# Kernel tuning notes

Measured on AMD Instinct MI355X. Metric: run time of the kernel, lower is better.

Reference implementation:

```python
import jax, jax.numpy as jnp
import numpy as np
from functools import partial

DG = 16          # deform groups
KH = KW = 3      # deformable kernel
K = KH * KW
MAX_MAG = 10.0   # max_residue_magnitude


def conv3x3(x, w, b):
    # x: [B,C,H,W], w: [O,C,3,3]
    y = jax.lax.conv_general_dilated(
        x, w, window_strides=(1, 1), padding=((1, 1), (1, 1)),
        dimension_numbers=('NCHW', 'OIHW', 'NCHW'))
    return y + b[None, :, None, None]


def lrelu(v):
    return jnp.where(v >= 0, v, 0.1 * v)


def modulated_deform_conv2d(x, offset, mask, weight, bias):
    """torchvision.ops.deform_conv2d semantics, stride=1, pad=1, dil=1, groups=1.
    x: [B,C,H,W]; offset: [B,2*DG*K,H,W] as (dy,dx) pairs; mask: [B,DG*K,H,W];
    weight: [Cout,C,KH,KW]; bias: [Cout]."""
    B, C, H, W = x.shape
    Cout = weight.shape[0]
    Ho, Wo = H, W  # stride 1, pad 1, 3x3
    Cp = C // DG

    off = offset.reshape(B, DG, K, 2, Ho, Wo)
    dy, dx = off[:, :, :, 0], off[:, :, :, 1]          # [B,DG,K,Ho,Wo]

    ki = (jnp.arange(K) // KW).astype(jnp.float32)      # kernel row
    kj = (jnp.arange(K) % KW).astype(jnp.float32)       # kernel col
    base_i = jnp.arange(Ho, dtype=jnp.float32) - 1.0    # i*stride - pad
    base_j = jnp.arange(Wo, dtype=jnp.float32) - 1.0
    py = dy + base_i[None, None, None, :, None] + ki[None, None, :, None, None]
    px = dx + base_j[None, None, None, None, :] + kj[None, None, :, None, None]

    y0 = jnp.floor(py)
    x0 = jnp.floor(px)
    wy = py - y0   # frac parts
    wx = px - x0
    y0i = y0.astype(jnp.int32)
    x0i = x0.astype(jnp.int32)

    xg = x.reshape(B, DG, Cp, H * W)
    P = K * Ho * Wo

    def gather(yi, xi, wgt):
        valid = (yi >= 0) & (yi < H) & (xi >= 0) & (xi < W)
        yc = jnp.clip(yi, 0, H - 1)
        xc = jnp.clip(xi, 0, W - 1)
        idx = (yc * W + xc).reshape(B, DG, 1, P)
        v = jnp.take_along_axis(xg, idx, axis=3)          # [B,DG,Cp,P]
        w = (wgt * valid.astype(x.dtype)).reshape(B, DG, 1, P)
        return v * w

    acc = gather(y0i,     x0i,     (1 - wy) * (1 - wx))
    acc = acc + gather(y0i,     x0i + 1, (1 - wy) * wx)
    acc = acc + gather(y0i + 1, x0i,     wy * (1 - wx))
    acc = acc + gather(y0i + 1, x0i + 1, wy * wx)

    acc = acc * mask.reshape(B, DG, 1, P)                 # modulation
    cols = acc.reshape(B, C, K, Ho * Wo)                  # [B,C,K,HW]
    out = jnp.einsum('ock,bckp->bop', weight.reshape(Cout, C, K), cols)
    out = out + bias[None, :, None]
    return out.reshape(B, Cout, Ho, Wo)


def forward(x, cond, flow, w1, b1, w2, b2, w3, b3, w4, b4, weight, bias):
    h = lrelu(conv3x3(cond, w1, b1))
    h = lrelu(conv3x3(h, w2, b2))
    h = lrelu(conv3x3(h, w3, b3))
    out = conv3x3(h, w4, b4)                              # [B,27*DG,H,W]
    offset, mask = out[:, :18 * DG], out[:, 18 * DG:]
    offset = MAX_MAG * jnp.tanh(offset)
    # flow channels are (dx,dy); flip -> (dy,dx) matching offset pair layout
    rep = offset.shape[1] // 2
    offset = offset + jnp.tile(flow[:, ::-1], (1, rep, 1, 1))
    mask = jax.nn.sigmoid(mask)
    return modulated_deform_conv2d(x, offset, mask, weight, bias)


def setup_inputs() -> dict:
    key = jax.random.key(0)
    ks = jax.random.split(key, 16)
    B, C, H, W = 2, 64, 128, 128
    Cc = 2 * C + 5  # 133
    s = 0.05
    return {
        'x': jax.random.normal(ks[0], (B, C, H, W), jnp.float32),
        'cond': jax.random.normal(ks[1], (B, Cc, H, W), jnp.float32),
        'flow': jax.random.normal(ks[2], (B, 2, H, W), jnp.float32),
        'w1': jax.random.normal(ks[3], (C, Cc, 3, 3), jnp.float32) * s,
        'b1': jax.random.normal(ks[4], (C,), jnp.float32) * s,
        'w2': jax.random.normal(ks[5], (C, C, 3, 3), jnp.float32) * s,
        'b2': jax.random.normal(ks[6], (C,), jnp.float32) * s,
        'w3': jax.random.normal(ks[7], (C, C, 3, 3), jnp.float32) * s,
        'b3': jax.random.normal(ks[8], (C,), jnp.float32) * s,
        'w4': jax.random.normal(ks[9], (27 * DG, C, 3, 3), jnp.float32) * s,
        'b4': jax.random.normal(ks[10], (27 * DG,), jnp.float32) * s,
        'weight': jax.random.normal(ks[11], (C, C, 3, 3), jnp.float32) * s,
        'bias': jax.random.normal(ks[12], (C,), jnp.float32) * s,
    }


def reference(x, cond, flow, w1, b1, w2, b2, w3, b3, w4, b4, weight, bias):
    return forward(x, cond, flow, w1, b1, w2, b2, w3, b3, w4, b4, weight, bias)
```

## Files before the change

### kernel.cpp

```cpp
#include <hip/hip_runtime.h>
#include <math.h>

#define Hh 128
#define Ww 128
#define HW (128*128)
#define PITCH 130
#define PADPX (130*130)

typedef unsigned short u16;
typedef unsigned int uint;
typedef _Float16 f16;
typedef __attribute__((ext_vector_type(8))) _Float16 f16x8;
typedef __attribute__((ext_vector_type(4))) _Float16 f16x4;
typedef __attribute__((ext_vector_type(4))) float f32x4;

__global__ __launch_bounds__(256) void zero_edge_k(u16* __restrict__ buf, int cu16) {
  int per_px = cu16 >> 3;
  int total = 516 * per_px;
  int idx = blockIdx.x * 256 + threadIdx.x;
  int b = blockIdx.y;
  if (idx >= total) return;
  int e = idx / per_px, q = idx - e * per_px;
  int y, x;
  if (e < 130)      { y = 0;   x = e; }
  else if (e < 260) { y = 129; x = e - 130; }
  else { int j = e - 260; y = 1 + (j >> 1); x = (j & 1) ? 129 : 0; }
  *(uint4*)&buf[((size_t)b * PADPX + (size_t)(y * PITCH + x)) * cu16 + q * 8] =
      make_uint4(0, 0, 0, 0);
}

__global__ __launch_bounds__(256) void prep_cond_k(const float* __restrict__ cond,
                                                   f16* __restrict__ out) {
  int p = blockIdx.x * 256 + threadIdx.x;
  int b = blockIdx.y;
  int y = p >> 7, x = p & 127;
  const float* cb = cond + (size_t)b * 133 * HW + p;
  f16* ob = out + ((size_t)b * PADPX + (size_t)((y + 1) * PITCH + x + 1)) * 160;
  for (int c = 0; c < 160; c += 8) {
    f16 buf[8];
    #pragma unroll
    for (int j = 0; j < 8; j++) {
      float v = (c + j < 133) ? cb[(size_t)(c + j) * HW] : 0.f;
      buf[j] = (f16)v;
    }
    *(uint4*)&ob[c] = *(uint4*)buf;
  }
}

__global__ __launch_bounds__(256) void wtrans_mfma_k(const float* __restrict__ w,
                                                     f16* __restrict__ wt,
                                                     int CIN, int NC, int NCOF) {
  int idx = blockIdx.x * 256 + threadIdx.x;
  int total = 9 * NC * NCOF * 64;
  if (idx >= total) return;
  int lane = idx & 63;
  int frag = idx >> 6;
  int f = frag % NCOF;
  int rest = frag / NCOF;
  int c = rest % NC;
  int t = rest / NC;
  int co = f * 16 + (lane & 15);
  int ci0 = c * 32 + (lane >> 4) * 8;
  f16 buf[8];
  #pragma unroll
  for (int j = 0; j < 8; j++) {
    int ci = ci0 + j;
    buf[j] = (f16)((ci < CIN) ? w[((size_t)co * CIN + ci) * 9 + t] : 0.f);
  }
  *(uint4*)&wt[(size_t)idx * 8] = *(uint4*)buf;
}

__global__ __launch_bounds__(256) void wtrans_dcn_mfma_k(const float* __restrict__ w,
                                                         f16* __restrict__ wt) {
  int idx = blockIdx.x * 256 + threadIdx.x;
  if (idx >= 18 * 4 * 64) return;
  int lane = idx & 63;
  int frag = idx >> 6;
  int f = frag & 3;
  int chunk = frag >> 2;
  int co = f * 16 + (lane & 15);
  int ci0 = chunk * 32 + (lane >> 4) * 8;
  f16 buf[8];
  #pragma unroll
  for (int j = 0; j < 8; j++) {
    int ci = ci0 + j;
    int k = ci >> 6, cig = ci & 63;
    buf[j] = (f16)w[((size_t)co * 64 + cig) * 9 + k];
  }
  *(uint4*)&wt[(size_t)idx * 8] = *(uint4*)buf;
}

__global__ __launch_bounds__(256) void xtrans2_k(const float* __restrict__ x,
                                                 f16* __restrict__ xt2, int B) {
  int idx = blockIdx.x * 256 + threadIdx.x;
  int total = B * 16 * HW;
  if (idx >= total) return;
  int b = idx / (16 * HW);
  int r = idx % (16 * HW);
  int dg = r / HW, p = r % HW;
  int y = p >> 7, xx = p & 127;
  int x1 = min(xx + 1, 127);
  const float* xb = x + ((size_t)b * 64 + dg * 4) * HW + (size_t)y * Ww;
  f16 o[8];
  #pragma unroll
  for (int c = 0; c < 4; c++) {
    o[c] = (f16)xb[(size_t)c * HW + xx];
    o[4 + c] = (f16)xb[(size_t)c * HW + x1];
  }
  *(uint4*)&xt2[(size_t)idx * 8] = *(uint4*)o;
}

template<int CINP, int NC, int NCF, int NCOF, int EPI>
__global__ __launch_bounds__(256) void conv_f16_k(
    const f16* __restrict__ in, const f16* __restrict__ wt,
    const float* __restrict__ bias, f16* __restrict__ out,
    float* __restrict__ offb, f16* __restrict__ mskb,
    const float* __restrict__ flow, int cogroups)
{
  __shared__ u16 lds[180 * 40];
  const int tid = threadIdx.x;
  const int lane = tid & 63, wave = tid >> 6;
  const int b = blockIdx.z / cogroups, cog = blockIdx.z % cogroups;
  const int gx0 = blockIdx.x * 16, gy0 = blockIdx.y * 8;

  f32x4 acc[2][NCF];
  #pragma unroll
  for (int i = 0; i < 2; i++)
    #pragma unroll
    for (int j = 0; j < NCF; j++) acc[i][j] = (f32x4)0.f;

  const f16* inb = in + (size_t)b * PADPX * CINP;

  for (int c = 0; c < NC; c++) {
    __syncthreads();
    for (int i = tid; i < 720; i += 256) {
      int pidx = i >> 2, q = i & 3;
      int py = pidx / 18, px = pidx - py * 18;
      size_t gp = (size_t)((gy0 + py) * PITCH + gx0 + px);
      uint4 v = *(const uint4*)&inb[gp * CINP + c * 32 + q * 8];
      *(uint4*)&lds[pidx * 40 + q * 8] = v;
    }
    __syncthreads();

    #pragma unroll
    for (int tap = 0; tap < 9; tap++) {
      const int dy = tap / 3, dx = tap % 3;
      f16x8 bfrag[2];
      #pragma unroll
      for (int pl = 0; pl < 2; pl++) {
        int pidx_r = (wave * 2 + pl + dy) * 18 + (lane & 15) + dx;
        bfrag[pl] = *(const f16x8*)&lds[pidx_r * 40 + (lane >> 4) * 8];
      }
      const f16* fA = wt + (((size_t)(tap * NC + c)) * NCOF + cog * NCF) * 512
                      + (size_t)lane * 8;
      #pragma unroll
      for (int cf = 0; cf < NCF; cf++) {
        f16x8 a = *(const f16x8*)&fA[(size_t)cf * 512];
        #pragma unroll
        for (int pl = 0; pl < 2; pl++)
          acc[pl][cf] = __builtin_amdgcn_mfma_f32_16x16x32_f16(a, bfrag[pl], acc[pl][cf], 0, 0, 0);
      }
    }
  }

  const int co_l = (lane >> 4) * 4;
  if (EPI == 0) {
    #pragma unroll
    for (int pl = 0; pl < 2; pl++) {
      size_t pp = (size_t)((gy0 + wave * 2 + pl + 1) * PITCH + gx0 + (lane & 15) + 1);
      f16* ob = out + ((size_t)b * PADPX + pp) * (NCOF * 16);
      #pragma unroll
      for (int cf = 0; cf < NCF; cf++) {
        int c0 = (cog * NCF + cf) * 16 + co_l;
        f16 buf[4];
        #pragma unroll
        for (int r = 0; r < 4; r++) {
          float v = acc[pl][cf][r] + bias[c0 + r];
          buf[r] = (f16)((v >= 0.f) ? v : 0.1f * v);
        }
        *(uint2*)&ob[c0] = *(uint2*)buf;
      }
    }
  } else {
    #pragma unroll
    for (int pl = 0; pl < 2; pl++) {
      size_t pix = (size_t)(gy0 + wave * 2 + pl) * Ww + gx0 + (lane & 15);
      float fl0 = flow[((size_t)b * 2 + 0) * HW + pix];
      float fl1 = flow[((size_t)b * 2 + 1) * HW + pix];
      #pragma unroll
      for (int cf = 0; cf < NCF; cf++) {
        int c0 = (cog * NCF + cf) * 16 + co_l;
        #pragma unroll
        for (int r = 0; r < 4; r++) {
          int cc = c0 + r;
          float v = acc[pl][cf][r] + bias[cc];
          if (cc < 288) {
            float e = __expf(2.f * v);
            float t = 1.f - 2.f * __builtin_amdgcn_rcpf(e + 1.f);
            offb[((size_t)b * 288 + cc) * HW + pix] = 10.f * t + ((cc & 1) ? fl0 : fl1);
          } else {
            mskb[((size_t)b * 144 + (cc - 288)) * HW + pix] =
                (f16)__builtin_amdgcn_rcpf(1.f + __expf(-v));
          }
        }
      }
    }
  }
}

__global__ __launch_bounds__(256) void dcn_fused_k(
    const f16* __restrict__ xt2, const float* __restrict__ off,
    const f16* __restrict__ msk, const f16* __restrict__ wtd,
    const float* __restrict__ bias, float* __restrict__ out)
{
  __shared__ u16 buf[2][64][72];
  const int tid = threadIdx.x;
  const int lane = tid & 63, wave = tid >> 6;
  const int bid = blockIdx.x;
  const int nid = (bid & 7) * 64 + (bid >> 3);
  const int b = nid >> 8;
  const int px0 = (nid & 255) * 64;
  const int pxl = tid & 63;
  const int px = px0 + pxl;
  const int y = px >> 7, x0i = px & 127;
  const int dg2 = tid >> 6;

  const float* offp = off + (size_t)b * 288 * HW + px;
  const f16*   mp   = msk + (size_t)b * 144 * HW + px;
  const f16*   xpl  = xt2 + (size_t)(b * 16 + dg2 * 4) * ((size_t)HW * 8);

  f32x4 acc[4];
  #pragma unroll
  for (int f = 0; f < 4; f++) acc[f] = (f32x4)0.f;

  float dyv[2][4], dxv[2][4], mvv[2][4];
  f16x8 g0[4], g1[4];
  float w00[4], w01[4], w10[4], w11[4];
  int hsel[4];

#define OFF_LOAD(kk, sl) { \
  _Pragma("unroll") \
  for (int i = 0; i < 4; i++) { int dg = dg2 * 4 + i; \
    dyv[sl][i] = offp[(size_t)(dg * 18 + 2 * (kk)) * HW]; \
    dxv[sl][i] = offp[(size_t)(dg * 18 + 2 * (kk) + 1) * HW]; \
    mvv[sl][i] = (float)mp[(size_t)(dg * 9 + (kk)) * HW]; } }

#define GATHER(kk, sl) { \
  _Pragma("unroll") \
  for (int i = 0; i < 4; i++) { \
    float py = (float)(y - 1 + (kk) / 3) + dyv[sl][i]; \
    float pxx = (float)(x0i - 1 + (kk) % 3) + dxv[sl][i]; \
    float y0f = floorf(py), x0f = floorf(pxx); \
    float wy = py - y0f, wx = pxx - x0f; \
    int yi = (int)y0f, xi = (int)x0f; \
    bool vy0 = (yi >= 0) & (yi < Hh); \
    bool vy1 = (yi + 1 >= 0) & (yi + 1 < Hh); \
    bool vx0 = (xi >= 0) & (xi < Ww); \
    bool vx1 = (xi + 1 >= 0) & (xi + 1 < Ww); \
    int y0c = min(max(yi, 0), Hh - 1), y1c = min(max(yi + 1, 0), Hh - 1); \
    int xb = min(max(xi, 0), Ww - 1); \
    hsel[i] = min(max(xi + 1, 0), Ww - 1) - xb; \
    float mv = mvv[sl][i]; \
    w00[i] = (vy0 && vx0) ? (1.f - wy) * (1.f - wx) * mv : 0.f; \
    w01[i] = (vy0 && vx1) ? (1.f - wy) * wx * mv : 0.f; \
    w10[i] = (vy1 && vx0) ? wy * (1.f - wx) * mv : 0.f; \
    w11[i] = (vy1 && vx1) ? wy * wx * mv : 0.f; \
    const f16* xp = xpl + (size_t)i * ((size_t)HW * 8); \
    g0[i] = *(const f16x8*)&xp[(size_t)(y0c * Ww + xb) * 8]; \
    g1[i] = *(const f16x8*)&xp[(size_t)(y1c * Ww + xb) * 8]; } }

#define FIN(nb) { \
  f16 o[16]; \
  _Pragma("unroll") \
  for (int i = 0; i < 4; i++) { \
    _Pragma("unroll") \
    for (int c = 0; c < 4; c++) { \
      float a00 = (float)g0[i][c]; \
      float a01 = hsel[i] ? (float)g0[i][4 + c] : (float)g0[i][c]; \
      float a10 = (float)g1[i][c]; \
      float a11 = hsel[i] ? (float)g1[i][4 + c] : (float)g1[i][c]; \
      o[i * 4 + c] = (f16)(a00 * w00[i] + a01 * w01[i] + a10 * w10[i] + a11 * w11[i]); } } \
  *(uint4*)&buf[nb][pxl][dg2 * 16] = *(uint4*)&o[0]; \
  *(uint4*)&buf[nb][pxl][dg2 * 16 + 8] = *(uint4*)&o[8]; }

#define MFMA_TAP(kk) { \
  _Pragma("unroll") \
  for (int ch = 0; ch < 2; ch++) { \
    f16x8 bfr = *(const f16x8*)&buf[(kk) & 1][wave * 16 + (lane & 15)][(lane >> 4) * 8 + ch * 32]; \
    const f16* wc = wtd + ((size_t)(((kk) * 2 + ch) * 4) * 64 + (size_t)lane) * 8; \
    _Pragma("unroll") \
    for (int f = 0; f < 4; f++) { \
      f16x8 a = *(const f16x8*)&wc[(size_t)f * 512]; \
      acc[f] = __builtin_amdgcn_mfma_f32_16x16x32_f16(a, bfr, acc[f], 0, 0, 0); } } }

  OFF_LOAD(0, 0);
  GATHER(0, 0);
  OFF_LOAD(1, 1);
  FIN(0);
  __syncthreads();

  #pragma unroll
  for (int k = 0; k < 9; k++) {
    if (k < 8) { GATHER(k + 1, (k + 1) & 1); }
    if (k < 7) { OFF_LOAD(k + 2, k & 1); }
    MFMA_TAP(k);
    if (k < 8) { FIN((k + 1) & 1); }
    __syncthreads();
  }

  const int pxo = px0 + wave * 16 + (lane & 15);
  #pragma unroll
  for (int f = 0; f < 4; f++) {
    #pragma unroll
    for (int r = 0; r < 4; r++) {
      int co = f * 16 + (lane >> 4) * 4 + r;
      out[((size_t)b * 64 + co) * HW + pxo] = acc[f][r] + bias[co];
    }
  }
#undef OFF_LOAD
#undef GATHER
#undef FIN
#undef MFMA_TAP
}

extern "C" void kernel_launch(void* const* d_in, const int* in_sizes, int n_in,
                              void* d_out, int out_size, void* d_ws, size_t ws_size,
                              hipStream_t stream) {
  const float* x    = (const float*)d_in[0];
  const float* cond = (const float*)d_in[1];
  const float* flow = (const float*)d_in[2];
  const float* w1 = (const float*)d_in[3];
  const float* b1 = (const float*)d_in[4];
  const float* w2 = (const float*)d_in[5];
  const float* b2 = (const float*)d_in[6];
  const float* w3 = (const float*)d_in[7];
  const float* b3 = (const float*)d_in[8];
  const float* w4 = (const float*)d_in[9];
  const float* b4 = (const float*)d_in[10];
  const float* wD = (const float*)d_in[11];
  const float* bD = (const float*)d_in[12];
  float* out = (float*)d_out;
  const int B = 2;

  char* ws = (char*)d_ws;
  f16* condp = (f16*)ws;
  f16* hA = (f16*)(ws + 10816000);
  f16* hB = (f16*)(ws + 15142400);
  char* pw = ws + 19468800;
  float* offb = (float*)pw;          pw += 37748736;
  f16*   mskb = (f16*)pw;            pw += 9437184;
  f16*   xt2  = (f16*)pw;            pw += 8388608;
  f16*   wt1  = (f16*)pw;            pw += 184320;
  f16*   wt2  = (f16*)pw;            pw += 73728;
  f16*   wt3  = (f16*)pw;            pw += 73728;
  f16*   wt4  = (f16*)pw;            pw += 497664;
  f16*   wtd  = (f16*)pw;            pw += 73728;

  zero_edge_k<<<dim3((516 * 20 + 255) / 256, B), 256, 0, stream>>>((u16*)condp, 160);
  zero_edge_k<<<dim3((516 * 8 + 255) / 256, B), 256, 0, stream>>>((u16*)hA, 64);
  zero_edge_k<<<dim3((516 * 8 + 255) / 256, B), 256, 0, stream>>>((u16*)hB, 64);
  prep_cond_k<<<dim3(HW / 256, B), 256, 0, stream>>>(cond, condp);
  xtrans2_k<<<dim3(B * 16 * HW / 256), 256, 0, stream>>>(x, xt2, B);
  wtrans_mfma_k<<<dim3((9 * 5 * 4 * 64 + 255) / 256), 256, 0, stream>>>(w1, wt1, 133, 5, 4);
  wtrans_mfma_k<<<dim3((9 * 2 * 4 * 64 + 255) / 256), 256, 0, stream>>>(w2, wt2, 64, 2, 4);
  wtrans_mfma_k<<<dim3((9 * 2 * 4 * 64 + 255) / 256), 256, 0, stream>>>(w3, wt3, 64, 2, 4);
  wtrans_mfma_k<<<dim3((9 * 2 * 27 * 64 + 255) / 256), 256, 0, stream>>>(w4, wt4, 64, 2, 27);
  wtrans_dcn_mfma_k<<<dim3((18 * 4 * 64 + 255) / 256), 256, 0, stream>>>(wD, wtd);

  conv_f16_k<160, 5, 1, 4, 0><<<dim3(8, 16, B * 4), 256, 0, stream>>>(
      condp, wt1, b1, hA, nullptr, nullptr, nullptr, 4);
  conv_f16_k<64, 2, 1, 4, 0><<<dim3(8, 16, B * 4), 256, 0, stream>>>(
      hA, wt2, b2, hB, nullptr, nullptr, nullptr, 4);
  conv_f16_k<64, 2, 1, 4, 0><<<dim3(8, 16, B * 4), 256, 0, stream>>>(
      hB, wt3, b3, hA, nullptr, nullptr, nullptr, 4);
  conv_f16_k<64, 2, 3, 27, 2><<<dim3(8, 16, B * 9), 256, 0, stream>>>(
      hA, wt4, b4, nullptr, offb, mskb, flow, 9);

  dcn_fused_k<<<dim3(512), 256, 0, stream>>>(xt2, offb, mskb, wtd, bD, out);
}
```

Baseline: 149.3 us.

## Prefetch conv input tiles into registers and repartition DCN over smaller pixel tiles

The conv kernel now loads the next channel chunk's input tile into registers while the current chunk is computed, then writes it to LDS after the barrier. This overlaps global-load latency with the MFMA work. The fused deformable conv is repartitioned so each block handles 16 pixels, with one thread per (pixel, deform group) and each wave owning 16 output channels. That gives 4x more blocks, fewer registers per thread and a higher occupancy hint. In exchange, each block reloads the DCN weights over fewer pixels, and the output stores become narrower.

```diff
diff --git a/kernel.cpp b/kernel.cpp
--- a/kernel.cpp
+++ b/kernel.cpp
@@ -131,15 +131,31 @@
 
   const f16* inb = in + (size_t)b * PADPX * CINP;
 
+  uint4 rbuf[3];
+#define LOADC(cc) { \
+    if (tid < 240) { \
+      _Pragma("unroll") \
+      for (int j = 0; j < 3; j++) { \
+        int i = j * 240 + tid; \
+        int pidx = i >> 2, q = i & 3; \
+        int py = pidx / 18, px = pidx - py * 18; \
+        size_t gp = (size_t)((gy0 + py) * PITCH + gx0 + px); \
+        rbuf[j] = *(const uint4*)&inb[gp * CINP + (cc) * 32 + q * 8]; \
+      } } }
+#define WRITEC() { \
+    if (tid < 240) { \
+      _Pragma("unroll") \
+      for (int j = 0; j < 3; j++) { \
+        int i = j * 240 + tid; \
+        int pidx = i >> 2, q = i & 3; \
+        *(uint4*)&lds[pidx * 40 + q * 8] = rbuf[j]; \
+      } } }
+
+  LOADC(0);
   for (int c = 0; c < NC; c++) {
     __syncthreads();
-    for (int i = tid; i < 720; i += 256) {
-      int pidx = i >> 2, q = i & 3;
-      int py = pidx / 18, px = pidx - py * 18;
-      size_t gp = (size_t)((gy0 + py) * PITCH + gx0 + px);
-      uint4 v = *(const uint4*)&inb[gp * CINP + c * 32 + q * 8];
-      *(uint4*)&lds[pidx * 40 + q * 8] = v;
-    }
+    WRITEC();
+    if (c + 1 < NC) LOADC(c + 1);
     __syncthreads();
 
     #pragma unroll
@@ -162,6 +178,8 @@
       }
     }
   }
+#undef LOADC
+#undef WRITEC
 
   const int co_l = (lane >> 4) * 4;
   if (EPI == 0) {
@@ -208,48 +226,42 @@
   }
 }
 
-__global__ __launch_bounds__(256) void dcn_fused_k(
+__global__ __launch_bounds__(256, 8) void dcn_fused_k(
     const f16* __restrict__ xt2, const float* __restrict__ off,
     const f16* __restrict__ msk, const f16* __restrict__ wtd,
     const float* __restrict__ bias, float* __restrict__ out)
 {
-  __shared__ u16 buf[2][64][72];
+  __shared__ u16 buf[2][16][72];
   const int tid = threadIdx.x;
   const int lane = tid & 63, wave = tid >> 6;
   const int bid = blockIdx.x;
-  const int nid = (bid & 7) * 64 + (bid >> 3);
-  const int b = nid >> 8;
-  const int px0 = (nid & 255) * 64;
-  const int pxl = tid & 63;
+  const int nid = (bid & 7) * 256 + (bid >> 3);
+  const int b = nid >> 10;
+  const int px0 = (nid & 1023) * 16;
+  const int pxl = tid & 15;
+  const int dg  = tid >> 4;
   const int px = px0 + pxl;
   const int y = px >> 7, x0i = px & 127;
-  const int dg2 = tid >> 6;
 
   const float* offp = off + (size_t)b * 288 * HW + px;
   const f16*   mp   = msk + (size_t)b * 144 * HW + px;
-  const f16*   xpl  = xt2 + (size_t)(b * 16 + dg2 * 4) * ((size_t)HW * 8);
-
-  f32x4 acc[4];
-  #pragma unroll
-  for (int f = 0; f < 4; f++) acc[f] = (f32x4)0.f;
-
-  float dyv[2][4], dxv[2][4], mvv[2][4];
-  f16x8 g0[4], g1[4];
-  float w00[4], w01[4], w10[4], w11[4];
-  int hsel[4];
+  const f16*   xp   = xt2 + (size_t)(b * 16 + dg) * ((size_t)HW * 8);
+
+  f32x4 acc = (f32x4)0.f;
+
+  float dyv[2], dxv[2], mvv[2];
+  f16x8 g0, g1;
+  float w00, w01, w10, w11;
+  int hsel;
 
 #define OFF_LOAD(kk, sl) { \
-  _Pragma("unroll") \
-  for (int i = 0; i < 4; i++) { int dg = dg2 * 4 + i; \
-    dyv[sl][i] = offp[(size_t)(dg * 18 + 2 * (kk)) * HW]; \
-    dxv[sl][i] = offp[(size_t)(dg * 18 + 2 * (kk) + 1) * HW]; \
-    mvv[sl][i] = (float)mp[(size_t)(dg * 9 + (kk)) * HW]; } }
+    dyv[sl] = offp[(size_t)(dg * 18 + 2 * (kk)) * HW]; \
+    dxv[sl] = offp[(size_t)(dg * 18 + 2 * (kk) + 1) * HW]; \
+    mvv[sl] = (float)mp[(size_t)(dg * 9 + (kk)) * HW]; }
 
 #define GATHER(kk, sl) { \
-  _Pragma("unroll") \
-  for (int i = 0; i < 4; i++) { \
-    float py = (float)(y - 1 + (kk) / 3) + dyv[sl][i]; \
-    float pxx = (float)(x0i - 1 + (kk) % 3) + dxv[sl][i]; \
+    float py = (float)(y - 1 + (kk) / 3) + dyv[sl]; \
+    float pxx = (float)(x0i - 1 + (kk) % 3) + dxv[sl]; \
     float y0f = floorf(py), x0f = floorf(pxx); \
     float wy = py - y0f, wx = pxx - x0f; \
     int yi = (int)y0f, xi = (int)x0f; \
@@ -259,39 +271,33 @@
     bool vx1 = (xi + 1 >= 0) & (xi + 1 < Ww); \
     int y0c = min(max(yi, 0), Hh - 1), y1c = min(max(yi + 1, 0), Hh - 1); \
     int xb = min(max(xi, 0), Ww - 1); \
-    hsel[i] = min(max(xi + 1, 0), Ww - 1) - xb; \
-    float mv = mvv[sl][i]; \
-    w00[i] = (vy0 && vx0) ? (1.f - wy) * (1.f - wx) * mv : 0.f; \
-    w01[i] = (vy0 && vx1) ? (1.f - wy) * wx * mv : 0.f; \
-    w10[i] = (vy1 && vx0) ? wy * (1.f - wx) * mv : 0.f; \
-    w11[i] = (vy1 && vx1) ? wy * wx * mv : 0.f; \
-    const f16* xp = xpl + (size_t)i * ((size_t)HW * 8); \
-    g0[i] = *(const f16x8*)&xp[(size_t)(y0c * Ww + xb) * 8]; \
-    g1[i] = *(const f16x8*)&xp[(size_t)(y1c * Ww + xb) * 8]; } }
+    hsel = min(max(xi + 1, 0), Ww - 1) - xb; \
+    float mv = mvv[sl]; \
+    w00 = (vy0 && vx0) ? (1.f - wy) * (1.f - wx) * mv : 0.f; \
+    w01 = (vy0 && vx1) ? (1.f - wy) * wx * mv : 0.f; \
+    w10 = (vy1 && vx0) ? wy * (1.f - wx) * mv : 0.f; \
+    w11 = (vy1 && vx1) ? wy * wx * mv : 0.f; \
+    g0 = *(const f16x8*)&xp[(size_t)(y0c * Ww + xb) * 8]; \
+    g1 = *(const f16x8*)&xp[(size_t)(y1c * Ww + xb) * 8]; }
 
 #define FIN(nb) { \
-  f16 o[16]; \
-  _Pragma("unroll") \
-  for (int i = 0; i < 4; i++) { \
+    f16 o[4]; \
     _Pragma("unroll") \
     for (int c = 0; c < 4; c++) { \
-      float a00 = (float)g0[i][c]; \
-      float a01 = hsel[i] ? (float)g0[i][4 + c] : (float)g0[i][c]; \
-      float a10 = (float)g1[i][c]; \
-      float a11 = hsel[i] ? (float)g1[i][4 + c] : (float)g1[i][c]; \
-      o[i * 4 + c] = (f16)(a00 * w00[i] + a01 * w01[i] + a10 * w10[i] + a11 * w11[i]); } } \
-  *(uint4*)&buf[nb][pxl][dg2 * 16] = *(uint4*)&o[0]; \
-  *(uint4*)&buf[nb][pxl][dg2 * 16 + 8] = *(uint4*)&o[8]; }
+      float a00 = (float)g0[c]; \
+      float a01 = hsel ? (float)g0[4 + c] : (float)g0[c]; \
+      float a10 = (float)g1[c]; \
+      float a11 = hsel ? (float)g1[4 + c] : (float)g1[c]; \
+      o[c] = (f16)(a00 * w00 + a01 * w01 + a10 * w10 + a11 * w11); } \
+    *(uint2*)&buf[nb][pxl][dg * 4] = *(uint2*)o; }
 
 #define MFMA_TAP(kk) { \
-  _Pragma("unroll") \
-  for (int ch = 0; ch < 2; ch++) { \
-    f16x8 bfr = *(const f16x8*)&buf[(kk) & 1][wave * 16 + (lane & 15)][(lane >> 4) * 8 + ch * 32]; \
-    const f16* wc = wtd + ((size_t)(((kk) * 2 + ch) * 4) * 64 + (size_t)lane) * 8; \
     _Pragma("unroll") \
-    for (int f = 0; f < 4; f++) { \
-      f16x8 a = *(const f16x8*)&wc[(size_t)f * 512]; \
-      acc[f] = __builtin_amdgcn_mfma_f32_16x16x32_f16(a, bfr, acc[f], 0, 0, 0); } } }
+    for (int ch = 0; ch < 2; ch++) { \
+      f16x8 bfr = *(const f16x8*)&buf[(kk) & 1][lane & 15][(lane >> 4) * 8 + ch * 32]; \
+      const f16* wc = wtd + ((size_t)((((kk) * 2 + ch) * 4 + wave)) * 64 + (size_t)lane) * 8; \
+      f16x8 a = *(const f16x8*)wc; \
+      acc = __builtin_amdgcn_mfma_f32_16x16x32_f16(a, bfr, acc, 0, 0, 0); } }
 
   OFF_LOAD(0, 0);
   GATHER(0, 0);
@@ -308,14 +314,11 @@
     __syncthreads();
   }
 
-  const int pxo = px0 + wave * 16 + (lane & 15);
-  #pragma unroll
-  for (int f = 0; f < 4; f++) {
-    #pragma unroll
-    for (int r = 0; r < 4; r++) {
-      int co = f * 16 + (lane >> 4) * 4 + r;
-      out[((size_t)b * 64 + co) * HW + pxo] = acc[f][r] + bias[co];
-    }
+  const int pxo = px0 + (lane & 15);
+  #pragma unroll
+  for (int r = 0; r < 4; r++) {
+    int co = wave * 16 + (lane >> 4) * 4 + r;
+    out[((size_t)b * 64 + co) * HW + pxo] = acc[r] + bias[co];
   }
 #undef OFF_LOAD
 #undef GATHER
@@ -376,5 +379,5 @@
   conv_f16_k<64, 2, 3, 27, 2><<<dim3(8, 16, B * 9), 256, 0, stream>>>(
       hA, wt4, b4, nullptr, offb, mskb, flow, 9);
 
-  dcn_fused_k<<<dim3(512), 256, 0, stream>>>(xt2, offb, mskb, wtd, bD, out);
-}
+  dcn_fused_k<<<dim3(2048), 256, 0, stream>>>(xt2, offb, mskb, wtd, bD, out);
+}
```

Result: slower. 187.0 us (+25.3%).

## Merge prep kernels into two launches and stage two channel chunks per sync

Applied to the files above, without the earlier changes.

Folds the edge-zeroing, cond and x transpose kernels into one prep launch, and the five weight-transform kernels into a second, cutting eight small launches. The conv kernel now loads two 32-channel chunks into shared memory per barrier pair, which halves the syncs for the 64-channel convs. The cost is double the LDS per block, which may lower occupancy, plus extra index arithmetic in the merged kernels.

```diff
diff --git a/kernel.cpp b/kernel.cpp
--- a/kernel.cpp
+++ b/kernel.cpp
@@ -11,113 +11,127 @@
 typedef unsigned int uint;
 typedef _Float16 f16;
 typedef __attribute__((ext_vector_type(8))) _Float16 f16x8;
-typedef __attribute__((ext_vector_type(4))) _Float16 f16x4;
 typedef __attribute__((ext_vector_type(4))) float f32x4;
 
-__global__ __launch_bounds__(256) void zero_edge_k(u16* __restrict__ buf, int cu16) {
-  int per_px = cu16 >> 3;
-  int total = 516 * per_px;
+__global__ __launch_bounds__(256) void prep_all_k(
+    const float* __restrict__ cond, const float* __restrict__ x,
+    f16* __restrict__ condp, f16* __restrict__ hA, f16* __restrict__ hB,
+    f16* __restrict__ xt2)
+{
+  int t = blockIdx.x * 256 + threadIdx.x;
+  if (t < 32768) {
+    int b = t >> 14, p = t & 16383;
+    int y = p >> 7, xx = p & 127;
+    const float* cb = cond + (size_t)b * 133 * HW + p;
+    f16* ob = condp + ((size_t)b * PADPX + (size_t)((y + 1) * PITCH + xx + 1)) * 160;
+    for (int c = 0; c < 160; c += 8) {
+      f16 buf[8];
+      #pragma unroll
+      for (int j = 0; j < 8; j++) {
+        float v = (c + j < 133) ? cb[(size_t)(c + j) * HW] : 0.f;
+        buf[j] = (f16)v;
+      }
+      *(uint4*)&ob[c] = *(uint4*)buf;
+    }
+    return;
+  }
+  t -= 32768;
+  if (t < 20640) {
+    int b = t / 10320, i = t % 10320;
+    int e = i / 20, q = i % 20;
+    int y, xx;
+    if (e < 130)      { y = 0;   xx = e; }
+    else if (e < 260) { y = 129; xx = e - 130; }
+    else { int j = e - 260; y = 1 + (j >> 1); xx = (j & 1) ? 129 : 0; }
+    *(uint4*)&condp[((size_t)b * PADPX + (size_t)(y * PITCH + xx)) * 160 + q * 8] =
+        make_uint4(0, 0, 0, 0);
+    return;
+  }
+  t -= 20640;
+  if (t < 16512) {
+    f16* buf = (t < 8256) ? hA : hB;
+    int i = t % 8256;
+    int b = i / 4128; i %= 4128;
+    int e = i / 8, q = i % 8;
+    int y, xx;
+    if (e < 130)      { y = 0;   xx = e; }
+    else if (e < 260) { y = 129; xx = e - 130; }
+    else { int j = e - 260; y = 1 + (j >> 1); xx = (j & 1) ? 129 : 0; }
+    *(uint4*)&buf[((size_t)b * PADPX + (size_t)(y * PITCH + xx)) * 64 + q * 8] =
+        make_uint4(0, 0, 0, 0);
+    return;
+  }
+  t -= 16512;
+  if (t < 524288) {
+    int b = t / (16 * HW);
+    int r = t % (16 * HW);
+    int dg = r / HW, p = r % HW;
+    int y = p >> 7, xx = p & 127;
+    int x1 = min(xx + 1, 127);
+    const float* xb = x + ((size_t)b * 64 + dg * 4) * HW + (size_t)y * Ww;
+    f16 o[8];
+    #pragma unroll
+    for (int c = 0; c < 4; c++) {
+      o[c] = (f16)xb[(size_t)c * HW + xx];
+      o[4 + c] = (f16)xb[(size_t)c * HW + x1];
+    }
+    *(uint4*)&xt2[(size_t)t * 8] = *(uint4*)o;
+  }
+}
+
+__global__ __launch_bounds__(256) void wtrans_all_k(
+    const float* __restrict__ w1, const float* __restrict__ w2,
+    const float* __restrict__ w3, const float* __restrict__ w4,
+    const float* __restrict__ wD,
+    f16* __restrict__ wt1, f16* __restrict__ wt2, f16* __restrict__ wt3,
+    f16* __restrict__ wt4, f16* __restrict__ wtd)
+{
   int idx = blockIdx.x * 256 + threadIdx.x;
-  int b = blockIdx.y;
-  if (idx >= total) return;
-  int e = idx / per_px, q = idx - e * per_px;
-  int y, x;
-  if (e < 130)      { y = 0;   x = e; }
-  else if (e < 260) { y = 129; x = e - 130; }
-  else { int j = e - 260; y = 1 + (j >> 1); x = (j & 1) ? 129 : 0; }
-  *(uint4*)&buf[((size_t)b * PADPX + (size_t)(y * PITCH + x)) * cu16 + q * 8] =
-      make_uint4(0, 0, 0, 0);
-}
-
-__global__ __launch_bounds__(256) void prep_cond_k(const float* __restrict__ cond,
-                                                   f16* __restrict__ out) {
-  int p = blockIdx.x * 256 + threadIdx.x;
-  int b = blockIdx.y;
-  int y = p >> 7, x = p & 127;
-  const float* cb = cond + (size_t)b * 133 * HW + p;
-  f16* ob = out + ((size_t)b * PADPX + (size_t)((y + 1) * PITCH + x + 1)) * 160;
-  for (int c = 0; c < 160; c += 8) {
+  if (idx >= 882 * 64) return;
+  int lane = idx & 63;
+  int fid = idx >> 6;
+  if (fid >= 810) {
+    int f2 = fid - 810;
+    int f = f2 & 3, chunk = f2 >> 2;
+    int co = f * 16 + (lane & 15);
+    int ci0 = chunk * 32 + (lane >> 4) * 8;
     f16 buf[8];
     #pragma unroll
     for (int j = 0; j < 8; j++) {
-      float v = (c + j < 133) ? cb[(size_t)(c + j) * HW] : 0.f;
-      buf[j] = (f16)v;
-    }
-    *(uint4*)&ob[c] = *(uint4*)buf;
-  }
-}
-
-__global__ __launch_bounds__(256) void wtrans_mfma_k(const float* __restrict__ w,
-                                                     f16* __restrict__ wt,
-                                                     int CIN, int NC, int NCOF) {
-  int idx = blockIdx.x * 256 + threadIdx.x;
-  int total = 9 * NC * NCOF * 64;
-  if (idx >= total) return;
-  int lane = idx & 63;
-  int frag = idx >> 6;
-  int f = frag % NCOF;
-  int rest = frag / NCOF;
+      int ci = ci0 + j;
+      buf[j] = (f16)wD[((size_t)co * 64 + (ci & 63)) * 9 + (ci >> 6)];
+    }
+    *(uint4*)&wtd[((size_t)f2 * 64 + lane) * 8] = *(uint4*)buf;
+    return;
+  }
+  const float* w; f16* wt; int CIN, NC, NCOF;
+  if (fid < 180)      { w = w1; wt = wt1; CIN = 133; NC = 5; NCOF = 4; }
+  else if (fid < 252) { w = w2; wt = wt2; CIN = 64; NC = 2; NCOF = 4; fid -= 180; }
+  else if (fid < 324) { w = w3; wt = wt3; CIN = 64; NC = 2; NCOF = 4; fid -= 252; }
+  else                { w = w4; wt = wt4; CIN = 64; NC = 2; NCOF = 27; fid -= 324; }
+  int f = fid % NCOF;
+  int rest = fid / NCOF;
   int c = rest % NC;
-  int t = rest / NC;
+  int tt = rest / NC;
   int co = f * 16 + (lane & 15);
   int ci0 = c * 32 + (lane >> 4) * 8;
   f16 buf[8];
   #pragma unroll
   for (int j = 0; j < 8; j++) {
     int ci = ci0 + j;
-    buf[j] = (f16)((ci < CIN) ? w[((size_t)co * CIN + ci) * 9 + t] : 0.f);
-  }
-  *(uint4*)&wt[(size_t)idx * 8] = *(uint4*)buf;
-}
-
-__global__ __launch_bounds__(256) void wtrans_dcn_mfma_k(const float* __restrict__ w,
-                                                         f16* __restrict__ wt) {
-  int idx = blockIdx.x * 256 + threadIdx.x;
-  if (idx >= 18 * 4 * 64) return;
-  int lane = idx & 63;
-  int frag = idx >> 6;
-  int f = frag & 3;
-  int chunk = frag >> 2;
-  int co = f * 16 + (lane & 15);
-  int ci0 = chunk * 32 + (lane >> 4) * 8;
-  f16 buf[8];
-  #pragma unroll
-  for (int j = 0; j < 8; j++) {
-    int ci = ci0 + j;
-    int k = ci >> 6, cig = ci & 63;
-    buf[j] = (f16)w[((size_t)co * 64 + cig) * 9 + k];
-  }
-  *(uint4*)&wt[(size_t)idx * 8] = *(uint4*)buf;
-}
-
-__global__ __launch_bounds__(256) void xtrans2_k(const float* __restrict__ x,
-                                                 f16* __restrict__ xt2, int B) {
-  int idx = blockIdx.x * 256 + threadIdx.x;
-  int total = B * 16 * HW;
-  if (idx >= total) return;
-  int b = idx / (16 * HW);
-  int r = idx % (16 * HW);
-  int dg = r / HW, p = r % HW;
-  int y = p >> 7, xx = p & 127;
-  int x1 = min(xx + 1, 127);
-  const float* xb = x + ((size_t)b * 64 + dg * 4) * HW + (size_t)y * Ww;
-  f16 o[8];
-  #pragma unroll
-  for (int c = 0; c < 4; c++) {
-    o[c] = (f16)xb[(size_t)c * HW + xx];
-    o[4 + c] = (f16)xb[(size_t)c * HW + x1];
-  }
-  *(uint4*)&xt2[(size_t)idx * 8] = *(uint4*)o;
-}
-
-template<int CINP, int NC, int NCF, int NCOF, int EPI>
+    buf[j] = (f16)((ci < CIN) ? w[((size_t)co * CIN + ci) * 9 + tt] : 0.f);
+  }
+  *(uint4*)&wt[((size_t)fid * 64 + lane) * 8] = *(uint4*)buf;
+}
+
+template<int CINP, int NC, int NCSTG, int NCF, int NCOF, int EPI>
 __global__ __launch_bounds__(256) void conv_f16_k(
     const f16* __restrict__ in, const f16* __restrict__ wt,
     const float* __restrict__ bias, f16* __restrict__ out,
     float* __restrict__ offb, f16* __restrict__ mskb,
     const float* __restrict__ flow, int cogroups)
 {
-  __shared__ u16 lds[180 * 40];
+  __shared__ u16 lds[NCSTG * 180 * 40];
   const int tid = threadIdx.x;
   const int lane = tid & 63, wave = tid >> 6;
   const int b = blockIdx.z / cogroups, cog = blockIdx.z % cogroups;
@@ -131,34 +145,40 @@
 
   const f16* inb = in + (size_t)b * PADPX * CINP;
 
-  for (int c = 0; c < NC; c++) {
+  for (int c0 = 0; c0 < NC; c0 += NCSTG) {
+    const int nch = (NC - c0 < NCSTG) ? (NC - c0) : NCSTG;
     __syncthreads();
-    for (int i = tid; i < 720; i += 256) {
-      int pidx = i >> 2, q = i & 3;
+    for (int i = tid; i < nch * 720; i += 256) {
+      int cc = i / 720, r = i - cc * 720;
+      int pidx = r >> 2, q = r & 3;
       int py = pidx / 18, px = pidx - py * 18;
       size_t gp = (size_t)((gy0 + py) * PITCH + gx0 + px);
-      uint4 v = *(const uint4*)&inb[gp * CINP + c * 32 + q * 8];
-      *(uint4*)&lds[pidx * 40 + q * 8] = v;
+      uint4 v = *(const uint4*)&inb[gp * CINP + (c0 + cc) * 32 + q * 8];
+      *(uint4*)&lds[cc * 7200 + pidx * 40 + q * 8] = v;
     }
     __syncthreads();
 
-    #pragma unroll
-    for (int tap = 0; tap < 9; tap++) {
-      const int dy = tap / 3, dx = tap % 3;
-      f16x8 bfrag[2];
+    for (int cl = 0; cl < NCSTG; cl++) {
+      if (c0 + cl >= NC) break;
+      const int c = c0 + cl;
       #pragma unroll
-      for (int pl = 0; pl < 2; pl++) {
-        int pidx_r = (wave * 2 + pl + dy) * 18 + (lane & 15) + dx;
-        bfrag[pl] = *(const f16x8*)&lds[pidx_r * 40 + (lane >> 4) * 8];
-      }
-      const f16* fA = wt + (((size_t)(tap * NC + c)) * NCOF + cog * NCF) * 512
-                      + (size_t)lane * 8;
-      #pragma unroll
-      for (int cf = 0; cf < NCF; cf++) {
-        f16x8 a = *(const f16x8*)&fA[(size_t)cf * 512];
+      for (int tap = 0; tap < 9; tap++) {
+        const int dy = tap / 3, dx = tap % 3;
+        f16x8 bfrag[2];
         #pragma unroll
-        for (int pl = 0; pl < 2; pl++)
-          acc[pl][cf] = __builtin_amdgcn_mfma_f32_16x16x32_f16(a, bfrag[pl], acc[pl][cf], 0, 0, 0);
+        for (int pl = 0; pl < 2; pl++) {
+          int pidx_r = (wave * 2 + pl + dy) * 18 + (lane & 15) + dx;
+          bfrag[pl] = *(const f16x8*)&lds[cl * 7200 + pidx_r * 40 + (lane >> 4) * 8];
+        }
+        const f16* fA = wt + (((size_t)(tap * NC + c)) * NCOF + cog * NCF) * 512
+                        + (size_t)lane * 8;
+        #pragma unroll
+        for (int cf = 0; cf < NCF; cf++) {
+          f16x8 a = *(const f16x8*)&fA[(size_t)cf * 512];
+          #pragma unroll
+          for (int pl = 0; pl < 2; pl++)
+            acc[pl][cf] = __builtin_amdgcn_mfma_f32_16x16x32_f16(a, bfrag[pl], acc[pl][cf], 0, 0, 0);
+        }
       }
     }
   }
@@ -356,24 +376,17 @@
   f16*   wt4  = (f16*)pw;            pw += 497664;
   f16*   wtd  = (f16*)pw;            pw += 73728;
 
-  zero_edge_k<<<dim3((516 * 20 + 255) / 256, B), 256, 0, stream>>>((u16*)condp, 160);
-  zero_edge_k<<<dim3((516 * 8 + 255) / 256, B), 256, 0, stream>>>((u16*)hA, 64);
-  zero_edge_k<<<dim3((516 * 8 + 255) / 256, B), 256, 0, stream>>>((u16*)hB, 64);
-  prep_cond_k<<<dim3(HW / 256, B), 256, 0, stream>>>(cond, condp);
-  xtrans2_k<<<dim3(B * 16 * HW / 256), 256, 0, stream>>>(x, xt2, B);
-  wtrans_mfma_k<<<dim3((9 * 5 * 4 * 64 + 255) / 256), 256, 0, stream>>>(w1, wt1, 133, 5, 4);
-  wtrans_mfma_k<<<dim3((9 * 2 * 4 * 64 + 255) / 256), 256, 0, stream>>>(w2, wt2, 64, 2, 4);
-  wtrans_mfma_k<<<dim3((9 * 2 * 4 * 64 + 255) / 256), 256, 0, stream>>>(w3, wt3, 64, 2, 4);
-  wtrans_mfma_k<<<dim3((9 * 2 * 27 * 64 + 255) / 256), 256, 0, stream>>>(w4, wt4, 64, 2, 27);
-  wtrans_dcn_mfma_k<<<dim3((18 * 4 * 64 + 255) / 256), 256, 0, stream>>>(wD, wtd);
-
-  conv_f16_k<160, 5, 1, 4, 0><<<dim3(8, 16, B * 4), 256, 0, stream>>>(
+  prep_all_k<<<dim3((594208 + 255) / 256), 256, 0, stream>>>(cond, x, condp, hA, hB, xt2);
+  wtrans_all_k<<<dim3((882 * 64 + 255) / 256), 256, 0, stream>>>(
+      w1, w2, w3, w4, wD, wt1, wt2, wt3, wt4, wtd);
+
+  conv_f16_k<160, 5, 2, 1, 4, 0><<<dim3(8, 16, B * 4), 256, 0, stream>>>(
       condp, wt1, b1, hA, nullptr, nullptr, nullptr, 4);
-  conv_f16_k<64, 2, 1, 4, 0><<<dim3(8, 16, B * 4), 256, 0, stream>>>(
+  conv_f16_k<64, 2, 2, 1, 4, 0><<<dim3(8, 16, B * 4), 256, 0, stream>>>(
       hA, wt2, b2, hB, nullptr, nullptr, nullptr, 4);
-  conv_f16_k<64, 2, 1, 4, 0><<<dim3(8, 16, B * 4), 256, 0, stream>>>(
+  conv_f16_k<64, 2, 2, 1, 4, 0><<<dim3(8, 16, B * 4), 256, 0, stream>>>(
       hB, wt3, b3, hA, nullptr, nullptr, nullptr, 4);
-  conv_f16_k<64, 2, 3, 27, 2><<<dim3(8, 16, B * 9), 256, 0, stream>>>(
+  conv_f16_k<64, 2, 2, 3, 27, 2><<<dim3(8, 16, B * 9), 256, 0, stream>>>(
       hA, wt4, b4, nullptr, offb, mskb, flow, 9);
 
   dcn_fused_k<<<dim3(512), 256, 0, stream>>>(xt2, offb, mskb, wtd, bD, out);
```

After: 127.8 us. 1.17x faster.
